# Kernel tuning notes

Hardware: AMD Instinct MI355X
Metric: run time of the kernel (lower is better)

Reference implementation:

```python
import jax, jax.numpy as jnp
import numpy as np

NEG = -1e30  # log-space 'zero'


def _lse3(a, b, c):
    # numerically stable logsumexp of three [B,L] arrays, NEG acts as -inf
    m = jnp.maximum(jnp.maximum(a, b), c)
    valid = m > NEG / 2
    m_safe = jnp.where(valid, m, 0.0)
    s = jnp.exp(a - m_safe) + jnp.exp(b - m_safe) + jnp.exp(c - m_safe)
    # add 1 where invalid so log() stays finite (result is masked anyway)
    return jnp.where(valid, m_safe + jnp.log(s + (~valid)), NEG)


def _lse2(a, b):
    m = jnp.maximum(a, b)
    valid = m > NEG / 2
    m_safe = jnp.where(valid, m, 0.0)
    s = jnp.exp(a - m_safe) + jnp.exp(b - m_safe)
    return jnp.where(valid, m_safe + jnp.log(s + (~valid)), NEG)


def ctc_loss(log_probs, targets, input_lengths, target_lengths):
    # log_probs: [T,B,C] already log-softmaxed; blank=0; reduction='mean'; zero_infinity
    T, B, C = log_probs.shape
    S = targets.shape[0] // B  # equal target lengths -> reshape concatenated targets
    tgt = targets.reshape(B, S)
    L = 2 * S + 1
    # extended label sequence: blank, l1, blank, l2, ..., blank
    ext = jnp.zeros((B, L), dtype=tgt.dtype).at[:, 1::2].set(tgt)
    # emissions gathered at extended labels: [T,B,L]
    emit = log_probs[:, jnp.arange(B)[:, None], ext]

    # skip transition (l-2 -> l) allowed iff ext[l] != blank and ext[l] != ext[l-2]
    skip_ok = jnp.concatenate(
        [jnp.zeros((B, 2), bool), (ext[:, 2:] != 0) & (ext[:, 2:] != ext[:, :-2])],
        axis=1,
    )

    def shift(a, n):
        return jnp.pad(a, ((0, 0), (n, 0)), constant_values=NEG)[:, :L]

    alpha0 = (
        jnp.full((B, L), NEG, log_probs.dtype)
        .at[:, 0].set(emit[0, :, 0])
        .at[:, 1].set(emit[0, :, 1])
    )

    def step(alpha, xs):
        t, emit_t = xs
        a1 = shift(alpha, 1)
        a2 = jnp.where(skip_ok, shift(alpha, 2), NEG)
        new = _lse3(alpha, a1, a2) + emit_t
        # freeze alpha once past each sample's input length
        new = jnp.where((t < input_lengths)[:, None], new, alpha)
        return new, None

    alpha, _ = jax.lax.scan(step, alpha0, (jnp.arange(1, T), emit[1:]))

    b_idx = jnp.arange(B)
    hi = 2 * target_lengths  # last blank position
    ll = _lse2(alpha[b_idx, hi], alpha[b_idx, hi - 1])
    loss = jnp.where(ll > NEG / 2, -ll, 0.0)  # zero_infinity=True
    return jnp.mean(loss / target_lengths.astype(log_probs.dtype))


def setup_inputs() -> dict:
    key = jax.random.key(0)
    k1, k2 = jax.random.split(key)
    T, B, C, S = 1024, 128, 256, 64
    logits = jax.random.normal(k1, (T, B, C), jnp.float32)
    log_probs = jax.nn.log_softmax(logits, axis=-1)
    targets = jax.random.randint(k2, (B * S,), 1, C)  # blank=0 excluded
    input_lengths = jnp.full((B,), T, jnp.int32)
    target_lengths = jnp.full((B,), S, jnp.int32)
    return {
        "log_probs": log_probs,
        "targets": targets,
        "input_lengths": input_lengths,
        "target_lengths": target_lengths,
    }


def reference(log_probs, targets, input_lengths, target_lengths):
    return ctc_loss(log_probs, targets, input_lengths, target_lengths)
```

## Files before the change

### kernel.cpp

```cpp
#include <hip/hip_runtime.h>


#define NEGV (-1e30f)
#define NEGH (-5e29f)

constexpr int T_  = 1024;
constexpr int C_  = 256;
constexpr int CH  = 64;
constexpr int NCH = T_ / CH;

__device__ __forceinline__ float lse2f(float x, float y) {
    float m = fmaxf(x, y);
    float s = __expf(x - m) + __expf(y - m);
    float r = m + __logf(s);
    return (m > NEGH) ? r : NEGV;
}

__device__ __forceinline__ double dshr1(double x) {
    int lo = __double2loint(x), hi = __double2hiint(x);
    int plo = __builtin_amdgcn_update_dpp(0, lo, 0x138, 0xf, 0xf, false);
    int phi = __builtin_amdgcn_update_dpp(0, hi, 0x138, 0xf, 0xf, false);
    return __hiloint2double(phi, plo);
}

template <int CTRL>
__device__ __forceinline__ int dpp_imaxstep(int x) {
    int r = __builtin_amdgcn_update_dpp(x, x, CTRL, 0xf, 0xf, false);
    return max(x, r);
}

#define PDECL(S) float S##g0,S##g1,S##g2,S##g3,S##g4,S##g5,S##g6,S##g7, \
                       S##l0,S##l1,S##l2,S##l3,S##l4,S##l5,S##l6,S##l7
#define PLOAD1(S,J,TB) { int t_ = (TB) + J; t_ = t_ > 1023 ? 1023 : t_;      \
    const float* rp_ = rowb + (size_t)t_ * BC;                               \
    S##g##J = rp_[my_tgt]; S##l##J = rp_[0]; }
#define PLOAD(S,TB) PLOAD1(S,0,TB) PLOAD1(S,1,TB) PLOAD1(S,2,TB)             \
                    PLOAD1(S,3,TB) PLOAD1(S,4,TB) PLOAD1(S,5,TB)             \
                    PLOAD1(S,6,TB) PLOAD1(S,7,TB)
#define PSTORE1(S,J,RB,BUFP) BUFP[((RB) + J) * 64 + lane] =                  \
    make_float2(__expf(S##g##J), __expf(S##l##J));
#define PSTORE(S,RB,BUFP) PSTORE1(S,0,RB,BUFP) PSTORE1(S,1,RB,BUFP)          \
                          PSTORE1(S,2,RB,BUFP) PSTORE1(S,3,RB,BUFP)          \
                          PSTORE1(S,4,RB,BUFP) PSTORE1(S,5,RB,BUFP)          \
                          PSTORE1(S,6,RB,BUFP) PSTORE1(S,7,RB,BUFP)
#define PRODUCE32(TSTART,RBASE,BUFP) {                                       \
    PDECL(A); PDECL(Bx);                                                     \
    PLOAD(A,  (TSTART));                                                     \
    PLOAD(Bx, (TSTART) + 8);                                                 \
    PSTORE(A,  (RBASE), BUFP);                                               \
    PLOAD(A,  (TSTART) + 16);                                                \
    PSTORE(Bx, (RBASE) + 8, BUFP);                                           \
    PLOAD(Bx, (TSTART) + 24);                                                \
    PSTORE(A,  (RBASE) + 16, BUFP);                                          \
    PSTORE(Bx, (RBASE) + 24, BUFP); }

__global__ __launch_bounds__(192) void ctc_alpha_kernel(
    const float* __restrict__ lp,
    const int* __restrict__ targets,
    const int* __restrict__ in_len,
    const int* __restrict__ tgt_len,
    float* __restrict__ partial,
    int B, int S)
{
    __shared__ float2 stage[2][CH * 64];
    __shared__ float sh[132];

    const int b    = blockIdx.x;
    const int tid  = threadIdx.x;
    const int wave = tid >> 6;
    const int lane = tid & 63;
    const int BC   = B * C_;
    const float* rowb = lp + (size_t)b * C_;

    int my_tgt = (lane < S) ? targets[b * S + lane] : 0;
    int prev_tgt = __shfl_up(my_tgt, 1);
    const bool skip = (lane > 0) && (my_tgt != prev_tgt) && (my_tgt != 0);
    const double skipd = skip ? 1.0 : 0.0;
    const int ilen = in_len[b];

    double pa = 0.0, pb = 0.0, pc = 0.0;
    int es = 0;
    if (wave == 0 && lane == 0) {
        pa = (double)__expf(rowb[0]);
        pb = (double)__expf(rowb[my_tgt]);
    }

    if (wave >= 1) {
        const int r0 = (wave - 1) * 32;
        float2* bp = &stage[0][0];
        PRODUCE32(1 + r0, r0, bp);
    }
    __syncthreads();

#define STEP(cur) {                                                          \
        double eml = (double)(cur).x;                                        \
        double ebl = (double)(cur).y;                                        \
        double pprev = dshr1(pb);                               \
        double u  = fma(skipd, pprev, pa);              \
        double nb = (pb + u) * eml;                          \
        double na = (pa + pprev) * ebl;                      \
        double nc = (pc + pb) * ebl;                         \
        pa = na; pb = nb; pc = nc; }

#define RESCALE() {                                                          \
        int h = max(max(__double2hiint(pa), __double2hiint(pb)),             \
                    __double2hiint(pc));                                     \
        h = dpp_imaxstep<0x111>(h);                         \
        h = dpp_imaxstep<0x112>(h);                         \
        h = dpp_imaxstep<0x114>(h);                         \
        h = dpp_imaxstep<0x118>(h);                         \
        h = dpp_imaxstep<0x142>(h);                         \
        h = dpp_imaxstep<0x143>(h);                         \
        int hm = __builtin_amdgcn_readlane(h, 63);                           \
        int e = ((hm >> 20) & 0x7ff) - 1023;                                 \
        pa = ldexp(pa, -e); pb = ldexp(pb, -e); pc = ldexp(pc, -e);          \
        es += e; }

    for (int kc = 0; kc < NCH; ++kc) {
        if (wave >= 1) {
            if (kc + 1 < NCH) {
                const int r0 = (wave - 1) * 32;
                const int t0 = 1 + (kc + 1) * CH + r0;
                float2* bp = &stage[(kc + 1) & 1][0];
                PRODUCE32(t0, r0, bp);
            }
        } else {
            const int t0 = 1 + kc * CH;
            const float2* sb = &stage[kc & 1][lane];
            if (t0 + CH <= ilen) {
                float2 f0 = sb[0 * 64];
                float2 f1 = sb[1 * 64];
                float2 f2 = sb[2 * 64];
                float2 f3 = sb[3 * 64];
#pragma unroll
                for (int r = 0; r < CH; ++r) {
                    float2 cur = f0;
                    f0 = f1; f1 = f2; f2 = f3;
                    if (r + 4 < CH) f3 = sb[(r + 4) * 64];
                    STEP(cur);
                    if ((r & 31) == 31) RESCALE();
                }
            } else if (t0 < ilen) {
                float2 f0 = sb[0 * 64];
                float2 f1 = sb[1 * 64];
                float2 f2 = sb[2 * 64];
                float2 f3 = sb[3 * 64];
#pragma unroll
                for (int r = 0; r < CH; ++r) {
                    float2 cur = f0;
                    f0 = f1; f1 = f2; f2 = f3;
                    if (r + 4 < CH) f3 = sb[(r + 4) * 64];
                    if (t0 + r < ilen) {
                        STEP(cur);
                        if ((r & 31) == 31) RESCALE();
                    }
                }
            }
        }
        __syncthreads();
    }

    if (wave == 0) {
        const double lses = (double)es * 0.6931471805599453;
        auto logp = [&](double p) -> float {
            if (p == 0.0) return NEGV;
            int hi = __double2hiint(p), lo = __double2loint(p);
            int E = ((hi >> 20) & 0x7ff) - 1023;
            int hin = (hi & (int)0x800FFFFF) | (1023 << 20);
            double m = __hiloint2double(hin, lo);
            return (float)(__logf((float)m) + ((double)E * 0.6931471805599453 + lses));
        };
        sh[2 * lane]     = logp(pa);
        sh[2 * lane + 1] = logp(pb);
        if (lane == 63) sh[128] = logp(pc);
    }
    __syncthreads();
    if (tid == 0) {
        int tl = tgt_len[b];
        int hi2 = 2 * tl;
        float ll = lse2f(sh[hi2], sh[hi2 - 1]);
        float loss = (ll > NEGH) ? -ll : 0.f;
        partial[b] = loss / (float)tl;
    }
}

__global__ __launch_bounds__(128) void ctc_reduce_kernel(
    const float* __restrict__ partial, float* __restrict__ out, int B)
{
    float v = 0.f;
    for (int j = threadIdx.x; j < B; j += 128) v += partial[j];
#pragma unroll
    for (int off = 32; off > 0; off >>= 1)
        v += __shfl_down(v, off);
    __shared__ float ws[2];
    if ((threadIdx.x & 63) == 0) ws[threadIdx.x >> 6] = v;
    __syncthreads();
    if (threadIdx.x == 0) out[0] = (ws[0] + ws[1]) / (float)B;
}

extern "C" void kernel_launch(void* const* d_in, const int* in_sizes, int n_in,
                              void* d_out, int out_size, void* d_ws, size_t ws_size,
                              hipStream_t stream)
{
    const float* lp      = (const float*)d_in[0];
    const int*   targets = (const int*)d_in[1];
    const int*   il      = (const int*)d_in[2];
    const int*   tl      = (const int*)d_in[3];
    const int B = in_sizes[2];
    const int S = in_sizes[1] / B;

    float* partial = (float*)d_ws;

    ctc_alpha_kernel<<<B, 192, 0, stream>>>(lp, targets, il, tl, partial, B, S);
    ctc_reduce_kernel<<<1, 128, 0, stream>>>(partial, (float*)d_out, B);
}
```

Before: 199.3 us.

## Run CTC alpha recursion in fp32 with frequent rescaling and deeper prefetch

Switches the scaled-probability alpha recursion from double to float, using a single DPP shift per step instead of two and a float-exponent rescale. To keep values in fp32 range, the rescale now runs every 8 steps instead of every 32. The producer waves now hold a full 32-row chunk in registers and load it one chunk ahead, so the global loads overlap the consumer's compute. This trades fp64 throughput for more rescale overhead, higher register pressure and some risk of precision loss or underflow on lanes whose values are far below the wave maximum.

```diff
diff --git a/kernel.cpp b/kernel.cpp
--- a/kernel.cpp
+++ b/kernel.cpp
@@ -16,11 +16,10 @@
     return (m > NEGH) ? r : NEGV;
 }
 
-__device__ __forceinline__ double dshr1(double x) {
-    int lo = __double2loint(x), hi = __double2hiint(x);
-    int plo = __builtin_amdgcn_update_dpp(0, lo, 0x138, 0xf, 0xf, false);
-    int phi = __builtin_amdgcn_update_dpp(0, hi, 0x138, 0xf, 0xf, false);
-    return __hiloint2double(phi, plo);
+__device__ __forceinline__ float fshr1(float x) {
+    int i = __float_as_int(x);
+    int p = __builtin_amdgcn_update_dpp(0, i, 0x138, 0xf, 0xf, false);
+    return __int_as_float(p);
 }
 
 template <int CTRL>
@@ -43,16 +42,10 @@
                           PSTORE1(S,2,RB,BUFP) PSTORE1(S,3,RB,BUFP)          \
                           PSTORE1(S,4,RB,BUFP) PSTORE1(S,5,RB,BUFP)          \
                           PSTORE1(S,6,RB,BUFP) PSTORE1(S,7,RB,BUFP)
-#define PRODUCE32(TSTART,RBASE,BUFP) {                                       \
-    PDECL(A); PDECL(Bx);                                                     \
-    PLOAD(A,  (TSTART));                                                     \
-    PLOAD(Bx, (TSTART) + 8);                                                 \
-    PSTORE(A,  (RBASE), BUFP);                                               \
-    PLOAD(A,  (TSTART) + 16);                                                \
-    PSTORE(Bx, (RBASE) + 8, BUFP);                                           \
-    PLOAD(Bx, (TSTART) + 24);                                                \
-    PSTORE(A,  (RBASE) + 16, BUFP);                                          \
-    PSTORE(Bx, (RBASE) + 24, BUFP); }
+#define LOADCHUNK(T0) PLOAD(A,(T0)) PLOAD(Bx,(T0)+8)                         \
+                      PLOAD(Cx,(T0)+16) PLOAD(Dx,(T0)+24)
+#define STORECHUNK(RB,BUFP) PSTORE(A,(RB),BUFP) PSTORE(Bx,(RB)+8,BUFP)       \
+                            PSTORE(Cx,(RB)+16,BUFP) PSTORE(Dx,(RB)+24,BUFP)
 
 __global__ __launch_bounds__(192) void ctc_alpha_kernel(
     const float* __restrict__ lp,
@@ -75,36 +68,37 @@
     int my_tgt = (lane < S) ? targets[b * S + lane] : 0;
     int prev_tgt = __shfl_up(my_tgt, 1);
     const bool skip = (lane > 0) && (my_tgt != prev_tgt) && (my_tgt != 0);
-    const double skipd = skip ? 1.0 : 0.0;
+    const float skipf = skip ? 1.f : 0.f;
     const int ilen = in_len[b];
 
-    double pa = 0.0, pb = 0.0, pc = 0.0;
+    float pa = 0.f, pb = 0.f, pc = 0.f;
     int es = 0;
-    if (wave == 0 && lane == 0) {
-        pa = (double)__expf(rowb[0]);
-        pb = (double)__expf(rowb[my_tgt]);
-    }
+
+    PDECL(A); PDECL(Bx); PDECL(Cx); PDECL(Dx);
+    const int r0 = (wave - 1) * 32;
 
     if (wave >= 1) {
-        const int r0 = (wave - 1) * 32;
-        float2* bp = &stage[0][0];
-        PRODUCE32(1 + r0, r0, bp);
+        LOADCHUNK(1 + r0);
+        { float2* bp = &stage[0][0]; STORECHUNK(r0, bp); }
+        LOADCHUNK(1 + CH + r0);
+    } else if (lane == 0) {
+        pa = __expf(rowb[0]);
+        pb = __expf(rowb[my_tgt]);
     }
     __syncthreads();
 
 #define STEP(cur) {                                                          \
-        double eml = (double)(cur).x;                                        \
-        double ebl = (double)(cur).y;                                        \
-        double pprev = dshr1(pb);                               \
-        double u  = fma(skipd, pprev, pa);              \
-        double nb = (pb + u) * eml;                          \
-        double na = (pa + pprev) * ebl;                      \
-        double nc = (pc + pb) * ebl;                         \
+        float eml = (cur).x;                                                 \
+        float ebl = (cur).y;                                                 \
+        float pprev = fshr1(pb);                                \
+        float t0s = pa + pb;                               \
+        float nb = fmaf(skipf, pprev, t0s) * eml;            \
+        float na = (pa + pprev) * ebl;                       \
+        float nc = (pc + pb) * ebl;                          \
         pa = na; pb = nb; pc = nc; }
 
 #define RESCALE() {                                                          \
-        int h = max(max(__double2hiint(pa), __double2hiint(pb)),             \
-                    __double2hiint(pc));                                     \
+        int h = __float_as_int(fmaxf(fmaxf(pa, pb), pc));                    \
         h = dpp_imaxstep<0x111>(h);                         \
         h = dpp_imaxstep<0x112>(h);                         \
         h = dpp_imaxstep<0x114>(h);                         \
@@ -112,17 +106,18 @@
         h = dpp_imaxstep<0x142>(h);                         \
         h = dpp_imaxstep<0x143>(h);                         \
         int hm = __builtin_amdgcn_readlane(h, 63);                           \
-        int e = ((hm >> 20) & 0x7ff) - 1023;                                 \
-        pa = ldexp(pa, -e); pb = ldexp(pb, -e); pc = ldexp(pc, -e);          \
+        int e = ((hm >> 23) & 0xff) - 127;                                   \
+        pa = ldexpf(pa, -e); pb = ldexpf(pb, -e); pc = ldexpf(pc, -e);       \
         es += e; }
 
     for (int kc = 0; kc < NCH; ++kc) {
         if (wave >= 1) {
             if (kc + 1 < NCH) {
-                const int r0 = (wave - 1) * 32;
-                const int t0 = 1 + (kc + 1) * CH + r0;
                 float2* bp = &stage[(kc + 1) & 1][0];
-                PRODUCE32(t0, r0, bp);
+                STORECHUNK(r0, bp);
+            }
+            if (kc + 2 < NCH) {
+                LOADCHUNK(1 + (kc + 2) * CH + r0);
             }
         } else {
             const int t0 = 1 + kc * CH;
@@ -138,7 +133,7 @@
                     f0 = f1; f1 = f2; f2 = f3;
                     if (r + 4 < CH) f3 = sb[(r + 4) * 64];
                     STEP(cur);
-                    if ((r & 31) == 31) RESCALE();
+                    if ((r & 7) == 7) RESCALE();
                 }
             } else if (t0 < ilen) {
                 float2 f0 = sb[0 * 64];
@@ -152,7 +147,7 @@
                     if (r + 4 < CH) f3 = sb[(r + 4) * 64];
                     if (t0 + r < ilen) {
                         STEP(cur);
-                        if ((r & 31) == 31) RESCALE();
+                        if ((r & 7) == 7) RESCALE();
                     }
                 }
             }
@@ -162,13 +157,14 @@
 
     if (wave == 0) {
         const double lses = (double)es * 0.6931471805599453;
-        auto logp = [&](double p) -> float {
-            if (p == 0.0) return NEGV;
-            int hi = __double2hiint(p), lo = __double2loint(p);
-            int E = ((hi >> 20) & 0x7ff) - 1023;
-            int hin = (hi & (int)0x800FFFFF) | (1023 << 20);
-            double m = __hiloint2double(hin, lo);
-            return (float)(__logf((float)m) + ((double)E * 0.6931471805599453 + lses));
+        auto logp = [&](float p) -> float {
+            if (p == 0.f) return NEGV;
+            float q = p * 33554432.0f;
+            if (q == 0.f) return NEGV;
+            int h = __float_as_int(q);
+            int E = ((h >> 23) & 0xff) - 127 - 25;
+            float m = __int_as_float((h & 0x807fffff) | (127 << 23));
+            return (float)(__logf(m) + ((double)E * 0.6931471805599453 + lses));
         };
         sh[2 * lane]     = logp(pa);
         sh[2 * lane + 1] = logp(pb);
```

New measurement: 195.1 us. 1.02x faster.
